# Optimization experiments

Hardware: AMD Instinct MI355X
Metric: run time of the kernel (lower is better)

Reference implementation:

```python
import jax, jax.numpy as jnp
import numpy as np

N_NODES = 100000
N_EDGES = 1600000
D_IN = 128
D_OUT = 128


def setup_inputs() -> dict:
    key = jax.random.key(0)
    k_x, k_e, k_wl, k_bl, k_wr = jax.random.split(key, 5)
    x = jax.random.normal(k_x, (N_NODES, D_IN), dtype=jnp.float32)
    edge_index = jax.random.randint(k_e, (2, N_EDGES), 0, N_NODES, dtype=jnp.int64)
    s = 1.0 / np.sqrt(D_IN)
    W_l = jax.random.uniform(k_wl, (D_OUT, D_IN), minval=-s, maxval=s, dtype=jnp.float32)
    b_l = jax.random.uniform(k_bl, (D_OUT,), minval=-s, maxval=s, dtype=jnp.float32)
    W_r = jax.random.uniform(k_wr, (D_OUT, D_IN), minval=-s, maxval=s, dtype=jnp.float32)
    return {"x": x, "edge_index": edge_index, "W_l": W_l, "b_l": b_l, "W_r": W_r}


def reference(x, edge_index, W_l, b_l, W_r):
    # PyG SAGEConv with mean aggregation:
    #   out = lin_l(mean_{j in N(i)} x_j) + lin_r(x_i), followed by ReLU.
    src, dst = edge_index[0], edge_index[1]
    # gather source features [E, D_IN] and mean-aggregate at destinations
    msg_sum = jax.ops.segment_sum(x[src], dst, num_segments=N_NODES)  # [N, D_IN]
    deg = jax.ops.segment_sum(jnp.ones((edge_index.shape[1],), dtype=x.dtype), dst,
                              num_segments=N_NODES)  # [N]
    agg = msg_sum / jnp.maximum(deg, 1.0)[:, None]  # isolated nodes -> 0
    out = agg @ W_l.T + b_l + x @ W_r.T
    return jax.nn.relu(out)
```

## Files before the change

### kernel.cpp

```cpp
#include <hip/hip_runtime.h>
#include <hip/hip_bf16.h>
#include <cstddef>
#include <cstdint>

#define D 128
#define BCHUNK 4096
#define SLOTS 64
#define QTILE 64
#define LROW 68
#define GRAN 512
#define SBCAP 9728
#define NGMAX 256
#define PSTRIDE 200
#define NBEMAX 416

typedef __bf16 bf16x8 __attribute__((ext_vector_type(8)));
typedef float  f32x4  __attribute__((ext_vector_type(4)));
typedef float  f32x2  __attribute__((ext_vector_type(2)));

__device__ __forceinline__ unsigned int f2bf(float f) {
    unsigned int u = __float_as_uint(f);
    return (u + 0x7FFFu + ((u >> 16) & 1u)) >> 16;
}

__global__ __launch_bounds__(256) void prep_kernel(
    const int* __restrict__ ei, int E, unsigned int* __restrict__ chunks,
    unsigned short* __restrict__ pref, int NG, int nbE, int nbX,
    const float4* __restrict__ x4, uint2* __restrict__ xb2,
    unsigned int* __restrict__ xg, int nq,
    const float* __restrict__ Wl, const float* __restrict__ Wr,
    const float* __restrict__ bl, unsigned short* __restrict__ bfrag,
    float* __restrict__ biasbuf)
{
    const int bid = blockIdx.x;
    if (bid >= nbE) {
        const int xi = bid - nbE;
        if (xi < nbX) {
            const int base = xi * 1024 + threadIdx.x;
            #pragma unroll
            for (int k = 0; k < 4; k++) {
                int i = base + k * 256;
                if (i < nq) {
                    float4 v = x4[i];
                    uint2 r;
                    r.x = f2bf(v.x) | (f2bf(v.y) << 16);
                    r.y = f2bf(v.z) | (f2bf(v.w) << 16);
                    xb2[i] = r;
                    int g = 0;
                    g = __builtin_amdgcn_cvt_pk_fp8_f32(v.x, v.y, g, false);
                    g = __builtin_amdgcn_cvt_pk_fp8_f32(v.z, v.w, g, true);
                    xg[(size_t)((i >> 5) + 1) * 32 + (i & 31)] = (unsigned int)g;
                }
            }
        } else {
            int f = (xi - nbX) * 256 + threadIdx.x;
            if (f < 4096) {
                int ct   = f >> 9;
                int q    = (f >> 6) & 7;
                int lane = f & 63;
                int o  = 16 * ct + (lane & 15);
                int kb = 32 * q + (lane >> 4) * 8;
                const float* s = (kb < 128) ? (Wl + (size_t)o * 128 + kb)
                                            : (Wr + (size_t)o * 128 + (kb - 128));
                uint4 u;
                u.x = f2bf(s[0]) | (f2bf(s[1]) << 16);
                u.y = f2bf(s[2]) | (f2bf(s[3]) << 16);
                u.z = f2bf(s[4]) | (f2bf(s[5]) << 16);
                u.w = f2bf(s[6]) | (f2bf(s[7]) << 16);
                reinterpret_cast<uint4*>(bfrag)[f] = u;
                if (f < 128) biasbuf[f] = bl[f];
                if (f < 32)  xg[f] = 0u;
            }
        }
        return;
    }
    __shared__ int cnt[NGMAX];
    __shared__ int wsum[4];
    __shared__ unsigned int ebuf[BCHUNK];

    for (int i = threadIdx.x; i < NG; i += 256) cnt[i] = 0;
    __syncthreads();
    const int cb = bid * BCHUNK;
    const int nE = min(E - cb, BCHUNK);
    int srcs[16], gs[16], d9s[16];
    #pragma unroll
    for (int k = 0; k < 16; k++) {
        int e = cb + threadIdx.x + k * 256;
        bool v = e < E;
        srcs[k] = v ? ei[e] : 0;
        int dst = v ? ei[E + e] : 0;
        gs[k]  = v ? (dst >> 9) : -1;
        d9s[k] = dst & 511;
        if (v) atomicAdd(&cnt[gs[k]], 1);
    }
    __syncthreads();
    const int tid = threadIdx.x;
    int c = (tid < NG) ? cnt[tid] : 0;
    int xsc = c;
    #pragma unroll
    for (int dd = 1; dd < 64; dd <<= 1) {
        int y = __shfl_up(xsc, dd);
        if ((tid & 63) >= dd) xsc += y;
    }
    if ((tid & 63) == 63) wsum[tid >> 6] = xsc;
    __syncthreads();
    int woff = 0;
    #pragma unroll
    for (int ww = 0; ww < 4; ww++)
        if (ww < (tid >> 6)) woff += wsum[ww];
    int pfx = xsc - c + woff;
    if (tid < NG)  pref[(size_t)bid * PSTRIDE + tid] = (unsigned short)pfx;
    if (tid == NG) pref[(size_t)bid * PSTRIDE + NG] = (unsigned short)nE;
    __syncthreads();
    if (tid < NG) cnt[tid] = pfx;
    __syncthreads();
    #pragma unroll
    for (int k = 0; k < 16; k++) {
        if (gs[k] >= 0) {
            int lp = atomicAdd(&cnt[gs[k]], 1);
            ebuf[lp] = (unsigned int)(srcs[k] + 1) | ((unsigned int)d9s[k] << 20);
        }
    }
    __syncthreads();
    unsigned int* dst = chunks + (size_t)bid * BCHUNK;
    #pragma unroll
    for (int p = 0; p < 4; p++) {
        int idx = p * 1024 + tid * 4;
        uint4 v = *reinterpret_cast<const uint4*>(&ebuf[idx]);
        *reinterpret_cast<uint4*>(&dst[idx]) = v;
    }
}

__global__ __launch_bounds__(512) void regroup_kernel(
    const unsigned int* __restrict__ chunks, const unsigned short* __restrict__ pref,
    int nbE, unsigned int* __restrict__ sub, int* __restrict__ subCnt, int NG)
{
    __shared__ int s_start[NBEMAX], s_off[NBEMAX], s_len[NBEMAX];
    __shared__ int wsumS[8];
    const int g    = blockIdx.x;
    const int tid  = threadIdx.x;
    const int w    = tid >> 6;
    const int lane = tid & 63;

    int st = 0, len = 0;
    if (tid < nbE) {
        st  = pref[(size_t)tid * PSTRIDE + g];
        len = pref[(size_t)tid * PSTRIDE + g + 1] - st;
    }
    int xsc = len;
    #pragma unroll
    for (int dd = 1; dd < 64; dd <<= 1) {
        int y = __shfl_up(xsc, dd);
        if (lane >= dd) xsc += y;
    }
    if (lane == 63) wsumS[w] = xsc;
    __syncthreads();
    int woff = 0;
    #pragma unroll
    for (int ww = 0; ww < 8; ww++)
        if (ww < w) woff += wsumS[ww];
    int off = xsc - len + woff;
    if (tid < nbE) { s_start[tid] = st; s_off[tid] = off; s_len[tid] = len; }
    if (tid == 511) subCnt[g] = off;
    __syncthreads();

    for (int b = w; b < nbE; b += 8) {
        int bst = s_start[b], boff = s_off[b], bln = s_len[b];
        const unsigned int* src = chunks + (size_t)b * BCHUNK + bst;
        for (int o = lane; o < bln; o += 64)
            if (boff + o < SBCAP) sub[(size_t)g * SBCAP + boff + o] = src[o];
    }
}

__global__ __launch_bounds__(512) void gathformer_kernel(
    const unsigned int* __restrict__ sub, const int* __restrict__ subCnt,
    const unsigned int* __restrict__ xg, const unsigned int* __restrict__ xb,
    const unsigned short* __restrict__ bfrag, const float* __restrict__ biasbuf,
    float* __restrict__ out, int N)
{
    __shared__ unsigned int lds[QTILE * LROW];
    __shared__ int lcsr[QTILE * SLOTS];
    __shared__ int lcnt[QTILE];

    const int g     = blockIdx.x >> 3;
    const int h     = blockIdx.x & 7;
    const int node0 = g * GRAN + (h << 6);

    const int w    = threadIdx.x >> 6;
    const int lane = threadIdx.x & 63;
    const int sb   = lane & 31;
    const int half = lane >> 5;

    if (threadIdx.x < QTILE) lcnt[threadIdx.x] = 0;
    __syncthreads();
    const int n = min(subCnt[g], SBCAP);
    const unsigned int* S = sub + (size_t)g * SBCAP;
    for (int bi = (int)threadIdx.x * 4; bi < n; bi += 2048) {
        uint4 e4 = *reinterpret_cast<const uint4*>(S + bi);
        #pragma unroll
        for (int j = 0; j < 4; j++) {
            unsigned int en = (&e4.x)[j];
            if (bi + j < n) {
                int d9 = (en >> 20) & 511;
                if ((d9 >> 6) == h) {
                    int ln  = d9 & 63;
                    int pos = atomicAdd(&lcnt[ln], 1);
                    if (pos < SLOTS) lcsr[ln * SLOTS + pos] = (int)(en & 0xFFFFFu);
                }
            }
        }
    }
    __syncthreads();

    const int imax = min(8, N - node0 - w * 8);
    #pragma unroll 2
    for (int i = 0; i < imax; i++) {
        int ln  = w * 8 + i;
        int deg = lcnt[ln];
        int dl  = min(deg, SLOTS);
        int nbatch = (dl + 15) >> 4;
        const int* nb = lcsr + ln * SLOTS;
        f32x2 a01 = {0.f, 0.f};
        f32x2 a23 = {0.f, 0.f};
        for (int b = 0; b < nbatch; b++) {
            const int j = b * 16;
            unsigned int v[8];
            #pragma unroll
            for (int u = 0; u < 8; u++) {
                int slot = j + 2 * u + half;
                int raw  = nb[slot];
                int s    = (slot < dl) ? raw : 0;
                v[u] = xg[(size_t)s * 32 + sb];
            }
            #pragma unroll
            for (int u = 0; u < 8; u++) {
                a01 += __builtin_amdgcn_cvt_pk_f32_fp8(v[u], false);
                a23 += __builtin_amdgcn_cvt_pk_f32_fp8(v[u], true);
            }
        }
        a01.x += __shfl_xor(a01.x, 32);
        a01.y += __shfl_xor(a01.y, 32);
        a23.x += __shfl_xor(a23.x, 32);
        a23.y += __shfl_xor(a23.y, 32);
        if (half == 0) {
            float inv = 1.0f / fmaxf((float)deg, 1.0f);
            int b = ln * LROW + sb * 2;
            lds[b]     = f2bf(a01.x * inv) | (f2bf(a01.y * inv) << 16);
            lds[b + 1] = f2bf(a23.x * inv) | (f2bf(a23.y * inv) << 16);
        }
    }
    __syncthreads();

    const int quad = lane >> 4;
    const int r15  = lane & 15;
    bf16x8 bw[8];
    #pragma unroll
    for (int q = 0; q < 8; q++)
        bw[q] = reinterpret_cast<const bf16x8*>(bfrag)[(w * 8 + q) * 64 + lane];
    const float bias = biasbuf[16 * w + r15];
    const int col = 16 * w + r15;

    #pragma unroll 1
    for (int mt = 0; mt < 4; mt++) {
        int rowbase = node0 + mt * 16;
        if (rowbase >= N) break;
        int rc = min(rowbase + r15, N - 1);
        f32x4 acc = {0.f, 0.f, 0.f, 0.f};
        const int lbase = (mt * 16 + r15) * LROW + quad * 4;
        #pragma unroll
        for (int q = 0; q < 4; q++) {
            bf16x8 a = *reinterpret_cast<const bf16x8*>(&lds[lbase + q * 16]);
            acc = __builtin_amdgcn_mfma_f32_16x16x32_bf16(a, bw[q], acc, 0, 0, 0);
        }
        const unsigned short* xrow =
            (const unsigned short*)xb + (size_t)rc * 128 + quad * 8;
        #pragma unroll
        for (int q = 4; q < 8; q++) {
            bf16x8 a = *reinterpret_cast<const bf16x8*>(xrow + (q - 4) * 32);
            acc = __builtin_amdgcn_mfma_f32_16x16x32_bf16(a, bw[q], acc, 0, 0, 0);
        }
        #pragma unroll
        for (int r = 0; r < 4; r++) {
            int orow = rowbase + quad * 4 + r;
            if (orow < N)
                out[(size_t)orow * D + col] = fmaxf(acc[r] + bias, 0.0f);
        }
    }
}

extern "C" void kernel_launch(void* const* d_in, const int* in_sizes, int n_in,
                              void* d_out, int out_size, void* d_ws, size_t ws_size,
                              hipStream_t stream)
{
    const float* x  = (const float*)d_in[0];
    const int*   ei = (const int*)d_in[1];
    const float* Wl = (const float*)d_in[2];
    const float* bl = (const float*)d_in[3];
    const float* Wr = (const float*)d_in[4];
    float* out = (float*)d_out;

    const int nodes = in_sizes[0] / D;
    const int E     = in_sizes[1] / 2;
    const int NG    = (nodes + GRAN - 1) / GRAN;
    const int nbE   = (E + BCHUNK - 1) / BCHUNK;

    unsigned int* xg = (unsigned int*)d_ws;
    unsigned int* xb = xg + (size_t)(nodes + 1) * 32;
    unsigned short* bfrag = (unsigned short*)(xb + (size_t)nodes * 64);
    float* biasbuf   = (float*)(bfrag + 4096 * 8);
    int* subCnt      = (int*)(biasbuf + 128);
    unsigned short* pref = (unsigned short*)(subCnt + 512);
    unsigned int* chunks = (unsigned int*)(pref + (size_t)nbE * PSTRIDE);
    unsigned int* sub    = chunks + (size_t)nbE * BCHUNK;

    const int nq  = nodes * 32;
    const int nbX = (nq + 1023) / 1024;
    prep_kernel<<<nbE + nbX + 16, 256, 0, stream>>>(
        ei, E, chunks, pref, NG, nbE, nbX,
        (const float4*)x, (uint2*)xb, xg, nq, Wl, Wr, bl, bfrag, biasbuf);

    regroup_kernel<<<NG, 512, 0, stream>>>(chunks, pref, nbE, sub, subCnt, NG);

    gathformer_kernel<<<NG * 8, 512, 0, stream>>>(
        sub, subCnt, xg, xb, bfrag, biasbuf, out, nodes);
}
```

Measured before the change: 206.8 us.

## Fold regroup pass into gather kernel, reading per-chunk runs directly

Measured after the change: 219.5 us. 1.06x slower.

```diff
diff --git a/kernel.cpp b/kernel.cpp
--- a/kernel.cpp
+++ b/kernel.cpp
@@ -9,7 +9,6 @@
 #define QTILE 64
 #define LROW 68
 #define GRAN 512
-#define SBCAP 9728
 #define NGMAX 256
 #define PSTRIDE 200
 #define NBEMAX 416
@@ -131,82 +130,46 @@
     }
 }
 
-__global__ __launch_bounds__(512) void regroup_kernel(
+__global__ __launch_bounds__(512) void gathformer_kernel(
     const unsigned int* __restrict__ chunks, const unsigned short* __restrict__ pref,
-    int nbE, unsigned int* __restrict__ sub, int* __restrict__ subCnt, int NG)
-{
-    __shared__ int s_start[NBEMAX], s_off[NBEMAX], s_len[NBEMAX];
-    __shared__ int wsumS[8];
-    const int g    = blockIdx.x;
-    const int tid  = threadIdx.x;
-    const int w    = tid >> 6;
-    const int lane = tid & 63;
-
-    int st = 0, len = 0;
-    if (tid < nbE) {
-        st  = pref[(size_t)tid * PSTRIDE + g];
-        len = pref[(size_t)tid * PSTRIDE + g + 1] - st;
-    }
-    int xsc = len;
-    #pragma unroll
-    for (int dd = 1; dd < 64; dd <<= 1) {
-        int y = __shfl_up(xsc, dd);
-        if (lane >= dd) xsc += y;
-    }
-    if (lane == 63) wsumS[w] = xsc;
-    __syncthreads();
-    int woff = 0;
-    #pragma unroll
-    for (int ww = 0; ww < 8; ww++)
-        if (ww < w) woff += wsumS[ww];
-    int off = xsc - len + woff;
-    if (tid < nbE) { s_start[tid] = st; s_off[tid] = off; s_len[tid] = len; }
-    if (tid == 511) subCnt[g] = off;
-    __syncthreads();
-
-    for (int b = w; b < nbE; b += 8) {
-        int bst = s_start[b], boff = s_off[b], bln = s_len[b];
-        const unsigned int* src = chunks + (size_t)b * BCHUNK + bst;
-        for (int o = lane; o < bln; o += 64)
-            if (boff + o < SBCAP) sub[(size_t)g * SBCAP + boff + o] = src[o];
-    }
-}
-
-__global__ __launch_bounds__(512) void gathformer_kernel(
-    const unsigned int* __restrict__ sub, const int* __restrict__ subCnt,
-    const unsigned int* __restrict__ xg, const unsigned int* __restrict__ xb,
+    int nbE, const unsigned int* __restrict__ xg, const unsigned int* __restrict__ xb,
     const unsigned short* __restrict__ bfrag, const float* __restrict__ biasbuf,
     float* __restrict__ out, int N)
 {
     __shared__ unsigned int lds[QTILE * LROW];
     __shared__ int lcsr[QTILE * SLOTS];
     __shared__ int lcnt[QTILE];
+    __shared__ unsigned int s_run[NBEMAX];
 
     const int g     = blockIdx.x >> 3;
     const int h     = blockIdx.x & 7;
     const int node0 = g * GRAN + (h << 6);
 
-    const int w    = threadIdx.x >> 6;
-    const int lane = threadIdx.x & 63;
+    const int tid  = threadIdx.x;
+    const int w    = tid >> 6;
+    const int lane = tid & 63;
     const int sb   = lane & 31;
     const int half = lane >> 5;
 
-    if (threadIdx.x < QTILE) lcnt[threadIdx.x] = 0;
-    __syncthreads();
-    const int n = min(subCnt[g], SBCAP);
-    const unsigned int* S = sub + (size_t)g * SBCAP;
-    for (int bi = (int)threadIdx.x * 4; bi < n; bi += 2048) {
-        uint4 e4 = *reinterpret_cast<const uint4*>(S + bi);
-        #pragma unroll
-        for (int j = 0; j < 4; j++) {
-            unsigned int en = (&e4.x)[j];
-            if (bi + j < n) {
-                int d9 = (en >> 20) & 511;
-                if ((d9 >> 6) == h) {
-                    int ln  = d9 & 63;
-                    int pos = atomicAdd(&lcnt[ln], 1);
-                    if (pos < SLOTS) lcsr[ln * SLOTS + pos] = (int)(en & 0xFFFFFu);
-                }
+    if (tid < QTILE) lcnt[tid] = 0;
+    for (int b = tid; b < nbE; b += 512) {
+        int st = pref[(size_t)b * PSTRIDE + g];
+        int en = pref[(size_t)b * PSTRIDE + g + 1];
+        s_run[b] = (unsigned int)st | ((unsigned int)(en - st) << 16);
+    }
+    __syncthreads();
+    for (int b = w; b < nbE; b += 8) {
+        unsigned int r = s_run[b];
+        int st = (int)(r & 0xFFFFu);
+        int ln = (int)(r >> 16);
+        const unsigned int* src = chunks + (size_t)b * BCHUNK + st;
+        for (int o = lane; o < ln; o += 64) {
+            unsigned int en = src[o];
+            int d9 = (en >> 20) & 511;
+            if ((d9 >> 6) == h) {
+                int nd  = d9 & 63;
+                int pos = atomicAdd(&lcnt[nd], 1);
+                if (pos < SLOTS) lcsr[nd * SLOTS + pos] = (int)(en & 0xFFFFFu);
             }
         }
     }
@@ -308,10 +271,8 @@
     unsigned int* xb = xg + (size_t)(nodes + 1) * 32;
     unsigned short* bfrag = (unsigned short*)(xb + (size_t)nodes * 64);
     float* biasbuf   = (float*)(bfrag + 4096 * 8);
-    int* subCnt      = (int*)(biasbuf + 128);
-    unsigned short* pref = (unsigned short*)(subCnt + 512);
-    unsigned int* chunks = (unsigned int*)(pref + (size_t)nbE * PSTRIDE);
-    unsigned int* sub    = chunks + (size_t)nbE * BCHUNK;
+    unsigned short* pref = (unsigned short*)(biasbuf + 128);
+    unsigned int* chunks = (unsigned int*)(pref + (size_t)nbE * PSTRIDE + 64);
 
     const int nq  = nodes * 32;
     const int nbX = (nq + 1023) / 1024;
@@ -319,8 +280,6 @@
         ei, E, chunks, pref, NG, nbE, nbX,
         (const float4*)x, (uint2*)xb, xg, nq, Wl, Wr, bl, bfrag, biasbuf);
 
-    regroup_kernel<<<NG, 512, 0, stream>>>(chunks, pref, nbE, sub, subCnt, NG);
-
     gathformer_kernel<<<NG * 8, 512, 0, stream>>>(
-        sub, subCnt, xg, xb, bfrag, biasbuf, out, nodes);
-}
+        chunks, pref, nbE, xg, xb, bfrag, biasbuf, out, nodes);
+}
```
